# Performance work log

Measured on AMD Instinct MI355X. Metric: run time of the kernel, lower is better.

Reference implementation:

```python
import jax, jax.numpy as jnp
import numpy as np

STATE_DIM = 8
ACTION_DIM = 2
HIDDEN = 16
N_NEIGHBORS = 16
NDATA = 262144


def setup_inputs() -> dict:
    key = jax.random.key(0)
    ks = jax.random.split(key, 9)
    sd, hl, ad, nn_ = STATE_DIM, HIDDEN, ACTION_DIM, N_NEIGHBORS
    return {
        "x": jax.random.normal(ks[0], (NDATA, sd * (1 + nn_)), dtype=jnp.float32),
        "phi_w1": jax.random.normal(ks[1], (32, sd), dtype=jnp.float32) * 0.1,
        "phi_b1": jax.random.normal(ks[2], (32,), dtype=jnp.float32) * 0.1,
        "phi_w2": jax.random.normal(ks[3], (hl, 32), dtype=jnp.float32) * 0.1,
        "phi_b2": jax.random.normal(ks[4], (hl,), dtype=jnp.float32) * 0.1,
        "rho_w1": jax.random.normal(ks[5], (32, sd + hl), dtype=jnp.float32) * 0.1,
        "rho_b1": jax.random.normal(ks[6], (32,), dtype=jnp.float32) * 0.1,
        "rho_w2": jax.random.normal(ks[7], (ad, 32), dtype=jnp.float32) * 0.1,
        "rho_b2": jax.random.normal(ks[8], (ad,), dtype=jnp.float32) * 0.1,
    }


def reference(x, phi_w1, phi_b1, phi_w2, phi_b2, rho_w1, rho_b1, rho_w2, rho_b2):
    nd = x.shape[0]
    sd, hl, nn_ = STATE_DIM, HIDDEN, N_NEIGHBORS
    s = x[:, :sd]                                   # [nd, sd] own state
    # unpack: reshape((state_dim, n_neighbors)) -> neighbor j is column j
    nb = x[:, sd:].reshape(nd, sd, nn_)             # [nd, sd, nn]
    nb = jnp.transpose(nb, (0, 2, 1)).reshape(nd * nn_, sd)  # [nd*nn, sd]
    # Phi over all neighbors (batched), then segment-sum by sample
    h = jax.nn.relu(nb @ phi_w1.T + phi_b1)         # [nd*nn, 32]
    h = jax.nn.relu(h @ phi_w2.T + phi_b2)          # [nd*nn, hl]
    summ = h.reshape(nd, nn_, hl).sum(axis=1)       # [nd, hl]
    X = jnp.concatenate([s, summ], axis=-1)         # [nd, sd+hl]
    # Rho
    y = jax.nn.relu(X @ rho_w1.T + rho_b1)          # [nd, 32]
    return jax.nn.relu(y @ rho_w2.T + rho_b2)       # [nd, action_dim]
```

## Files before the change

### kernel.cpp

```cpp
#include <hip/hip_runtime.h>

#define NDATA 262144
#define SD 8
#define HL 16
#define NN 16
#define ROWLEN (SD * (1 + NN))

__global__ __launch_bounds__(256) void deepset_kernel(
    const float* __restrict__ x,
    const float* __restrict__ phi_w1, const float* __restrict__ phi_b1,
    const float* __restrict__ phi_w2, const float* __restrict__ phi_b2,
    const float* __restrict__ rho_w1, const float* __restrict__ rho_b1,
    const float* __restrict__ rho_w2, const float* __restrict__ rho_b2,
    float* __restrict__ out)
{
    const int tid = blockIdx.x * blockDim.x + threadIdx.x;
    const int row = tid >> 4;
    const int j   = tid & 15;
    const float* __restrict__ xr = x + (long)row * ROWLEN;

    float nb[SD];
#pragma unroll
    for (int d = 0; d < SD; ++d)
        nb[d] = xr[SD + d * NN + j];

    float h1[32];
#pragma unroll
    for (int o = 0; o < 32; ++o) {
        float acc = phi_b1[o];
#pragma unroll
        for (int d = 0; d < SD; ++d)
            acc = fmaf(phi_w1[o * SD + d], nb[d], acc);
        h1[o] = fmaxf(acc, 0.0f);
    }

    float h2[HL];
#pragma unroll
    for (int k = 0; k < HL; ++k) {
        float acc = phi_b2[k];
#pragma unroll
        for (int o = 0; o < 32; ++o)
            acc = fmaf(phi_w2[k * 32 + o], h1[o], acc);
        h2[k] = fmaxf(acc, 0.0f);
    }

#pragma unroll
    for (int k = 0; k < HL; ++k) {
#pragma unroll
        for (int m = 1; m < 16; m <<= 1)
            h2[k] += __shfl_xor(h2[k], m);
    }

    const int o0 = 2 * j;
    float y0 = rho_b1[o0 + 0];
    float y1 = rho_b1[o0 + 1];
    const float* __restrict__ w0 = rho_w1 + (o0 + 0) * (SD + HL);
    const float* __restrict__ w1 = rho_w1 + (o0 + 1) * (SD + HL);
#pragma unroll
    for (int d = 0; d < SD; ++d) {
        const float sv = xr[d];
        y0 = fmaf(w0[d], sv, y0);
        y1 = fmaf(w1[d], sv, y1);
    }
#pragma unroll
    for (int k = 0; k < HL; ++k) {
        y0 = fmaf(w0[SD + k], h2[k], y0);
        y1 = fmaf(w1[SD + k], h2[k], y1);
    }
    y0 = fmaxf(y0, 0.0f);
    y1 = fmaxf(y1, 0.0f);

    float p0 = fmaf(rho_w2[0 * 32 + o0], y0, rho_w2[0 * 32 + o0 + 1] * y1);
    float p1 = fmaf(rho_w2[1 * 32 + o0], y0, rho_w2[1 * 32 + o0 + 1] * y1);
#pragma unroll
    for (int m = 1; m < 16; m <<= 1) {
        p0 += __shfl_xor(p0, m);
        p1 += __shfl_xor(p1, m);
    }

    if (j == 0) {
        float2 r;
        r.x = fmaxf(p0 + rho_b2[0], 0.0f);
        r.y = fmaxf(p1 + rho_b2[1], 0.0f);
        reinterpret_cast<float2*>(out)[row] = r;
    }
}

extern "C" void kernel_launch(void* const* d_in, const int* in_sizes, int n_in,
                              void* d_out, int out_size, void* d_ws, size_t ws_size,
                              hipStream_t stream) {
    const float* x      = (const float*)d_in[0];
    const float* phi_w1 = (const float*)d_in[1];
    const float* phi_b1 = (const float*)d_in[2];
    const float* phi_w2 = (const float*)d_in[3];
    const float* phi_b2 = (const float*)d_in[4];
    const float* rho_w1 = (const float*)d_in[5];
    const float* rho_b1 = (const float*)d_in[6];
    const float* rho_w2 = (const float*)d_in[7];
    const float* rho_b2 = (const float*)d_in[8];
    float* out = (float*)d_out;

    const int threads = 256;
    const int total   = NDATA * NN;
    const int blocks  = total / threads;

    deepset_kernel<<<blocks, threads, 0, stream>>>(
        x, phi_w1, phi_b1, phi_w2, phi_b2,
        rho_w1, rho_b1, rho_w2, rho_b2, out);
}
```

Baseline: 269.8 us.

## Process four rows per thread group and reduce with DPP row rotations

Each 16-lane group now handles four samples instead of one. This reuses every phi/rho weight load across four rows and fuses the two phi layers, so the 32-wide hidden array is no longer materialised. The shfl_xor reductions, which go through ds_bpermute, are replaced by DPP row_ror adds that all-reduce within 16-lane rows. The trade is higher register pressure (64 accumulators plus neighbor values per thread) and a quarter as many threads.

```diff
diff --git a/kernel.cpp b/kernel.cpp
--- a/kernel.cpp
+++ b/kernel.cpp
@@ -5,6 +5,20 @@
 #define HL 16
 #define NN 16
 #define ROWLEN (SD * (1 + NN))
+#define RPG 4
+
+__device__ __forceinline__ float group_allreduce(float v) {
+    int t;
+    t = __builtin_amdgcn_update_dpp(0, __float_as_int(v), 0x128, 0xF, 0xF, true);
+    v += __int_as_float(t);
+    t = __builtin_amdgcn_update_dpp(0, __float_as_int(v), 0x124, 0xF, 0xF, true);
+    v += __int_as_float(t);
+    t = __builtin_amdgcn_update_dpp(0, __float_as_int(v), 0x122, 0xF, 0xF, true);
+    v += __int_as_float(t);
+    t = __builtin_amdgcn_update_dpp(0, __float_as_int(v), 0x121, 0xF, 0xF, true);
+    v += __int_as_float(t);
+    return v;
+}
 
 __global__ __launch_bounds__(256) void deepset_kernel(
     const float* __restrict__ x,
@@ -15,74 +29,114 @@
     float* __restrict__ out)
 {
     const int tid = blockIdx.x * blockDim.x + threadIdx.x;
-    const int row = tid >> 4;
+    const int g   = tid >> 4;
     const int j   = tid & 15;
-    const float* __restrict__ xr = x + (long)row * ROWLEN;
+    const long row0 = (long)g * RPG;
+    const float* __restrict__ xr0 = x + row0 * ROWLEN;
 
-    float nb[SD];
+    float nb[RPG][SD];
 #pragma unroll
-    for (int d = 0; d < SD; ++d)
-        nb[d] = xr[SD + d * NN + j];
+    for (int r = 0; r < RPG; ++r)
+#pragma unroll
+        for (int d = 0; d < SD; ++d)
+            nb[r][d] = xr0[r * ROWLEN + SD + d * NN + j];
 
-    float h1[32];
+    float acc[RPG][HL];
+#pragma unroll
+    for (int r = 0; r < RPG; ++r)
+#pragma unroll
+        for (int k = 0; k < HL; ++k)
+            acc[r][k] = 0.0f;
+
 #pragma unroll
     for (int o = 0; o < 32; ++o) {
-        float acc = phi_b1[o];
+        const float b1 = phi_b1[o];
+        float t[RPG];
 #pragma unroll
-        for (int d = 0; d < SD; ++d)
-            acc = fmaf(phi_w1[o * SD + d], nb[d], acc);
-        h1[o] = fmaxf(acc, 0.0f);
-    }
-
-    float h2[HL];
+        for (int r = 0; r < RPG; ++r) t[r] = b1;
 #pragma unroll
-    for (int k = 0; k < HL; ++k) {
-        float acc = phi_b2[k];
+        for (int d = 0; d < SD; ++d) {
+            const float w = phi_w1[o * SD + d];
 #pragma unroll
-        for (int o = 0; o < 32; ++o)
-            acc = fmaf(phi_w2[k * 32 + o], h1[o], acc);
-        h2[k] = fmaxf(acc, 0.0f);
+            for (int r = 0; r < RPG; ++r)
+                t[r] = fmaf(w, nb[r][d], t[r]);
+        }
+#pragma unroll
+        for (int r = 0; r < RPG; ++r) t[r] = fmaxf(t[r], 0.0f);
+#pragma unroll
+        for (int k = 0; k < HL; ++k) {
+            const float w = phi_w2[k * 32 + o];
+#pragma unroll
+            for (int r = 0; r < RPG; ++r)
+                acc[r][k] = fmaf(w, t[r], acc[r][k]);
+        }
     }
 
 #pragma unroll
     for (int k = 0; k < HL; ++k) {
+        const float b2 = phi_b2[k];
 #pragma unroll
-        for (int m = 1; m < 16; m <<= 1)
-            h2[k] += __shfl_xor(h2[k], m);
+        for (int r = 0; r < RPG; ++r)
+            acc[r][k] = group_allreduce(fmaxf(acc[r][k] + b2, 0.0f));
     }
 
+    float sv[RPG][SD];
+#pragma unroll
+    for (int r = 0; r < RPG; ++r)
+#pragma unroll
+        for (int d = 0; d < SD; ++d)
+            sv[r][d] = xr0[r * ROWLEN + d];
+
     const int o0 = 2 * j;
-    float y0 = rho_b1[o0 + 0];
-    float y1 = rho_b1[o0 + 1];
     const float* __restrict__ w0 = rho_w1 + (o0 + 0) * (SD + HL);
     const float* __restrict__ w1 = rho_w1 + (o0 + 1) * (SD + HL);
+    float y0[RPG], y1[RPG];
+    {
+        const float bb0 = rho_b1[o0 + 0];
+        const float bb1 = rho_b1[o0 + 1];
+#pragma unroll
+        for (int r = 0; r < RPG; ++r) { y0[r] = bb0; y1[r] = bb1; }
+    }
 #pragma unroll
     for (int d = 0; d < SD; ++d) {
-        const float sv = xr[d];
-        y0 = fmaf(w0[d], sv, y0);
-        y1 = fmaf(w1[d], sv, y1);
+        const float a0 = w0[d];
+        const float a1 = w1[d];
+#pragma unroll
+        for (int r = 0; r < RPG; ++r) {
+            y0[r] = fmaf(a0, sv[r][d], y0[r]);
+            y1[r] = fmaf(a1, sv[r][d], y1[r]);
+        }
     }
 #pragma unroll
     for (int k = 0; k < HL; ++k) {
-        y0 = fmaf(w0[SD + k], h2[k], y0);
-        y1 = fmaf(w1[SD + k], h2[k], y1);
+        const float a0 = w0[SD + k];
+        const float a1 = w1[SD + k];
+#pragma unroll
+        for (int r = 0; r < RPG; ++r) {
+            y0[r] = fmaf(a0, acc[r][k], y0[r]);
+            y1[r] = fmaf(a1, acc[r][k], y1[r]);
+        }
     }
-    y0 = fmaxf(y0, 0.0f);
-    y1 = fmaxf(y1, 0.0f);
-
-    float p0 = fmaf(rho_w2[0 * 32 + o0], y0, rho_w2[0 * 32 + o0 + 1] * y1);
-    float p1 = fmaf(rho_w2[1 * 32 + o0], y0, rho_w2[1 * 32 + o0 + 1] * y1);
 #pragma unroll
-    for (int m = 1; m < 16; m <<= 1) {
-        p0 += __shfl_xor(p0, m);
-        p1 += __shfl_xor(p1, m);
+    for (int r = 0; r < RPG; ++r) {
+        y0[r] = fmaxf(y0[r], 0.0f);
+        y1[r] = fmaxf(y1[r], 0.0f);
     }
 
-    if (j == 0) {
-        float2 r;
-        r.x = fmaxf(p0 + rho_b2[0], 0.0f);
-        r.y = fmaxf(p1 + rho_b2[1], 0.0f);
-        reinterpret_cast<float2*>(out)[row] = r;
+    const float z00 = rho_w2[0 * 32 + o0], z01 = rho_w2[0 * 32 + o0 + 1];
+    const float z10 = rho_w2[1 * 32 + o0], z11 = rho_w2[1 * 32 + o0 + 1];
+    const float rb0 = rho_b2[0], rb1 = rho_b2[1];
+
+#pragma unroll
+    for (int r = 0; r < RPG; ++r) {
+        float p0 = group_allreduce(fmaf(z00, y0[r], z01 * y1[r]));
+        float p1 = group_allreduce(fmaf(z10, y0[r], z11 * y1[r]));
+        if (j == 0) {
+            float2 res;
+            res.x = fmaxf(p0 + rb0, 0.0f);
+            res.y = fmaxf(p1 + rb1, 0.0f);
+            reinterpret_cast<float2*>(out)[row0 + r] = res;
+        }
     }
 }
 
@@ -101,8 +155,8 @@
     float* out = (float*)d_out;
 
     const int threads = 256;
-    const int total   = NDATA * NN;
-    const int blocks  = total / threads;
+    const long total  = (long)NDATA / RPG * 16;
+    const int blocks  = (int)(total / threads);
 
     deepset_kernel<<<blocks, threads, 0, stream>>>(
         x, phi_w1, phi_b1, phi_w2, phi_b2,
```

After: 273.2 us. About the same (+1.3%).

## Compute phi MLP with bf16 MFMA and DPP reductions, batching rows per wave

Applied to the files above, without the earlier changes.

Replaces the per-thread scalar FMA evaluation of the phi network with two layers of 32x32x16 bf16 MFMA instructions. The first layer's bias is folded into the K dimension, and permlane32 swaps re-layout the hidden activations between layers. Each wave now processes 32 rows across several iterations, staging the neighbor sums in LDS for the rho stage and using DPP row reductions in place of shuffles. This targets the heavy FP32 ALU cost of the phi layers but lowers precision to bf16 for inputs and weights, which may affect accuracy tolerance.

```diff
diff --git a/kernel.cpp b/kernel.cpp
--- a/kernel.cpp
+++ b/kernel.cpp
@@ -4,7 +4,41 @@
 #define SD 8
 #define HL 16
 #define NN 16
-#define ROWLEN (SD * (1 + NN))
+#define ROWLEN 136
+#define NB 4
+
+typedef __attribute__((ext_vector_type(8)))  short bf16x8;
+typedef __attribute__((ext_vector_type(16))) float f32x16;
+
+__device__ __forceinline__ unsigned short f2bf(float f) {
+    unsigned u = __float_as_uint(f);
+    return (unsigned short)((u + 0x7FFFu + ((u >> 16) & 1u)) >> 16);
+}
+__device__ __forceinline__ unsigned pk2(float lo, float hi) {
+    return (unsigned)f2bf(lo) | ((unsigned)f2bf(hi) << 16);
+}
+__device__ __forceinline__ unsigned cvtpk(float a, float b) {
+    unsigned r;
+    asm("v_cvt_pk_bf16_f32 %0, %1, %2" : "=v"(r) : "v"(a), "v"(b));
+    return r;
+}
+__device__ __forceinline__ void plswap(unsigned &a, unsigned &b) {
+    asm volatile("v_permlane32_swap_b32 %0, %1" : "+v"(a), "+v"(b));
+}
+union FragU { unsigned u[4]; bf16x8 v; };
+
+__device__ __forceinline__ float group_allreduce(float v) {
+    int t;
+    t = __builtin_amdgcn_update_dpp(0, __float_as_int(v), 0x128, 0xF, 0xF, true);
+    v += __int_as_float(t);
+    t = __builtin_amdgcn_update_dpp(0, __float_as_int(v), 0x124, 0xF, 0xF, true);
+    v += __int_as_float(t);
+    t = __builtin_amdgcn_update_dpp(0, __float_as_int(v), 0x122, 0xF, 0xF, true);
+    v += __int_as_float(t);
+    t = __builtin_amdgcn_update_dpp(0, __float_as_int(v), 0x121, 0xF, 0xF, true);
+    v += __int_as_float(t);
+    return v;
+}
 
 __global__ __launch_bounds__(256) void deepset_kernel(
     const float* __restrict__ x,
@@ -14,75 +48,133 @@
     const float* __restrict__ rho_w2, const float* __restrict__ rho_b2,
     float* __restrict__ out)
 {
-    const int tid = blockIdx.x * blockDim.x + threadIdx.x;
-    const int row = tid >> 4;
-    const int j   = tid & 15;
-    const float* __restrict__ xr = x + (long)row * ROWLEN;
-
-    float nb[SD];
-#pragma unroll
-    for (int d = 0; d < SD; ++d)
-        nb[d] = xr[SD + d * NN + j];
-
-    float h1[32];
-#pragma unroll
-    for (int o = 0; o < 32; ++o) {
-        float acc = phi_b1[o];
-#pragma unroll
-        for (int d = 0; d < SD; ++d)
-            acc = fmaf(phi_w1[o * SD + d], nb[d], acc);
-        h1[o] = fmaxf(acc, 0.0f);
+    __shared__ float lds_summ[4][8][16];
+
+    const int lane = threadIdx.x & 63;
+    const int w    = threadIdx.x >> 6;
+    const int h    = lane >> 5;
+    const int n31  = lane & 31;
+    const int c    = n31 & 15;
+    const int p    = n31 >> 4;
+
+    FragU a1;
+    if (h == 0) {
+        const float* wr = phi_w1 + n31 * SD;
+        a1.u[0] = pk2(wr[0], wr[1]);
+        a1.u[1] = pk2(wr[2], wr[3]);
+        a1.u[2] = pk2(wr[4], wr[5]);
+        a1.u[3] = pk2(wr[6], wr[7]);
+    } else {
+        a1.u[0] = pk2(phi_b1[n31], 0.0f);
+        a1.u[1] = 0u; a1.u[2] = 0u; a1.u[3] = 0u;
     }
 
-    float h2[HL];
-#pragma unroll
-    for (int k = 0; k < HL; ++k) {
-        float acc = phi_b2[k];
-#pragma unroll
-        for (int o = 0; o < 32; ++o)
-            acc = fmaf(phi_w2[k * 32 + o], h1[o], acc);
-        h2[k] = fmaxf(acc, 0.0f);
+    FragU b2[2];
+#pragma unroll
+    for (int kt = 0; kt < 2; ++kt) {
+        const float* wr = phi_w2 + (n31 & 15) * 32 + 16 * kt + 8 * h;
+#pragma unroll
+        for (int q = 0; q < 4; ++q) {
+            float e0 = (n31 < HL) ? wr[2 * q]     : 0.0f;
+            float e1 = (n31 < HL) ? wr[2 * q + 1] : 0.0f;
+            b2[kt].u[q] = pk2(e0, e1);
+        }
     }
-
-#pragma unroll
-    for (int k = 0; k < HL; ++k) {
-#pragma unroll
-        for (int m = 1; m < 16; m <<= 1)
-            h2[k] += __shfl_xor(h2[k], m);
-    }
-
-    const int o0 = 2 * j;
-    float y0 = rho_b1[o0 + 0];
-    float y1 = rho_b1[o0 + 1];
-    const float* __restrict__ w0 = rho_w1 + (o0 + 0) * (SD + HL);
-    const float* __restrict__ w1 = rho_w1 + (o0 + 1) * (SD + HL);
-#pragma unroll
-    for (int d = 0; d < SD; ++d) {
-        const float sv = xr[d];
-        y0 = fmaf(w0[d], sv, y0);
-        y1 = fmaf(w1[d], sv, y1);
-    }
-#pragma unroll
-    for (int k = 0; k < HL; ++k) {
-        y0 = fmaf(w0[SD + k], h2[k], y0);
-        y1 = fmaf(w1[SD + k], h2[k], y1);
-    }
-    y0 = fmaxf(y0, 0.0f);
-    y1 = fmaxf(y1, 0.0f);
-
-    float p0 = fmaf(rho_w2[0 * 32 + o0], y0, rho_w2[0 * 32 + o0 + 1] * y1);
-    float p1 = fmaf(rho_w2[1 * 32 + o0], y0, rho_w2[1 * 32 + o0 + 1] * y1);
-#pragma unroll
-    for (int m = 1; m < 16; m <<= 1) {
-        p0 += __shfl_xor(p0, m);
-        p1 += __shfl_xor(p1, m);
-    }
-
-    if (j == 0) {
-        float2 r;
-        r.x = fmaxf(p0 + rho_b2[0], 0.0f);
-        r.y = fmaxf(p1 + rho_b2[1], 0.0f);
-        reinterpret_cast<float2*>(out)[row] = r;
+    const float b2v = phi_b2[n31 & 15];
+
+    const long gw = (long)blockIdx.x * 4 + w;
+
+    for (int b = 0; b < NB; ++b) {
+        const long rbase = gw * (8 * NB) + (long)b * 8;
+
+#pragma unroll
+        for (int t = 0; t < 4; ++t) {
+            const long row = rbase + 2 * t + p;
+            const float* xb = x + (size_t)row * ROWLEN + SD + c;
+
+            float f0 = xb[0 * NN], f1 = xb[1 * NN], f2 = xb[2 * NN], f3 = xb[3 * NN];
+            float f4 = xb[4 * NN], f5 = xb[5 * NN], f6 = xb[6 * NN], f7 = xb[7 * NN];
+            FragU b1;
+            b1.u[0] = h ? 0x00003F80u : cvtpk(f0, f1);
+            b1.u[1] = h ? 0u          : cvtpk(f2, f3);
+            b1.u[2] = h ? 0u          : cvtpk(f4, f5);
+            b1.u[3] = h ? 0u          : cvtpk(f6, f7);
+
+            f32x16 z = {0,0,0,0,0,0,0,0,0,0,0,0,0,0,0,0};
+            f32x16 d1 = __builtin_amdgcn_mfma_f32_32x32x16_bf16(a1.v, b1.v, z, 0, 0, 0);
+
+            float r[16];
+#pragma unroll
+            for (int i = 0; i < 16; ++i) r[i] = fmaxf(d1[i], 0.0f);
+
+            FragU a2[2];
+#pragma unroll
+            for (int kt = 0; kt < 2; ++kt) {
+                unsigned wa0 = cvtpk(r[8 * kt + 0], r[8 * kt + 1]);
+                unsigned wa1 = cvtpk(r[8 * kt + 2], r[8 * kt + 3]);
+                unsigned wb0 = cvtpk(r[8 * kt + 4], r[8 * kt + 5]);
+                unsigned wb1 = cvtpk(r[8 * kt + 6], r[8 * kt + 7]);
+                plswap(wa0, wb0);
+                plswap(wa1, wb1);
+                a2[kt].u[0] = wa0; a2[kt].u[1] = wa1;
+                a2[kt].u[2] = wb0; a2[kt].u[3] = wb1;
+            }
+
+            f32x16 d2 = __builtin_amdgcn_mfma_f32_32x32x16_bf16(a2[0].v, b2[0].v, z, 0, 0, 0);
+            d2 = __builtin_amdgcn_mfma_f32_32x32x16_bf16(a2[1].v, b2[1].v, d2, 0, 0, 0);
+
+            float s0 = 0.0f, s1 = 0.0f;
+#pragma unroll
+            for (int i = 0; i < 8; ++i) {
+                s0 += fmaxf(d2[i] + b2v, 0.0f);
+                s1 += fmaxf(d2[8 + i] + b2v, 0.0f);
+            }
+            s0 += __shfl_xor(s0, 32);
+            s1 += __shfl_xor(s1, 32);
+
+            if (n31 < HL)
+                lds_summ[w][2 * t + h][n31] = h ? s1 : s0;
+        }
+
+#pragma unroll
+        for (int it = 0; it < 2; ++it) {
+            const int  lrow = it * 4 + (lane >> 4);
+            const long row  = rbase + lrow;
+            const int  j16  = lane & 15;
+            const float* xr = x + (size_t)row * ROWLEN;
+            const float* sm = &lds_summ[w][lrow][0];
+
+            const int o0 = 2 * j16;
+            const float* w0  = rho_w1 + (size_t)o0 * (SD + HL);
+            const float* w1r = w0 + (SD + HL);
+            float y0 = rho_b1[o0], y1 = rho_b1[o0 + 1];
+#pragma unroll
+            for (int d = 0; d < SD; ++d) {
+                const float sv = xr[d];
+                y0 = fmaf(w0[d],  sv, y0);
+                y1 = fmaf(w1r[d], sv, y1);
+            }
+#pragma unroll
+            for (int k = 0; k < HL; ++k) {
+                const float s = sm[k];
+                y0 = fmaf(w0[SD + k],  s, y0);
+                y1 = fmaf(w1r[SD + k], s, y1);
+            }
+            y0 = fmaxf(y0, 0.0f);
+            y1 = fmaxf(y1, 0.0f);
+
+            float p0 = fmaf(rho_w2[o0],      y0, rho_w2[o0 + 1]      * y1);
+            float p1 = fmaf(rho_w2[32 + o0], y0, rho_w2[32 + o0 + 1] * y1);
+            p0 = group_allreduce(p0);
+            p1 = group_allreduce(p1);
+
+            if (j16 == 0) {
+                float2 res;
+                res.x = fmaxf(p0 + rho_b2[0], 0.0f);
+                res.y = fmaxf(p1 + rho_b2[1], 0.0f);
+                reinterpret_cast<float2*>(out)[row] = res;
+            }
+        }
     }
 }
 
@@ -100,11 +192,9 @@
     const float* rho_b2 = (const float*)d_in[8];
     float* out = (float*)d_out;
 
-    const int threads = 256;
-    const int total   = NDATA * NN;
-    const int blocks  = total / threads;
-
-    deepset_kernel<<<blocks, threads, 0, stream>>>(
+    const int blocks = NDATA / (4 * 8 * NB);
+
+    deepset_kernel<<<blocks, 256, 0, stream>>>(
         x, phi_w1, phi_b1, phi_w2, phi_b2,
         rho_w1, rho_b1, rho_w2, rho_b2, out);
 }
```

Result: faster. 252.9 us (-6.2%).
